# Kernel optimization log

Hardware: AMD Instinct MI355X
Metric: run time of the kernel (lower is better)

Reference implementation:

```python
import jax, jax.numpy as jnp
import numpy as np

NHEADS = 16
SCALE_BASE = 512
GN_EPS = 1e-5


def rotate_every_two(x):
    x1 = x[..., ::2]
    x2 = x[..., 1::2]
    return jnp.stack((-x2, x1), axis=-1).reshape(x.shape)


def xpos_apply(x, downscale, offset=0):
    # x: [B, T, C]; XPOS over the FULL embedding dim (applied before head split)
    B, T, C = x.shape
    half = C // 2
    scale_vec = (jnp.arange(0, C, 2, dtype=jnp.float32) + 0.4 * C) / (1.4 * C)  # [half]
    min_pos = -(T + offset) // 2
    max_pos = T + offset + min_pos
    power = jnp.arange(min_pos, max_pos, dtype=jnp.float32) / SCALE_BASE  # [L]
    scale = scale_vec[None, :] ** power[:, None]  # [L, half]
    L = scale.shape[0]
    inv_freq = 1.0 / (10000.0 ** (jnp.arange(half, dtype=jnp.float32) / half))
    sinusoid = jnp.arange(L, dtype=jnp.float32)[:, None] * inv_freq[None, :]  # [L, half]
    sin, cos = jnp.sin(sinusoid), jnp.cos(sinusoid)
    if L > T:
        scale, sin, cos = scale[-T:], sin[-T:], cos[-T:]
    if downscale:
        scale = 1.0 / scale
    sin = jnp.repeat(sin * scale, 2, axis=-1)  # [T, C] (duplicate_interleave)
    cos = jnp.repeat(cos * scale, 2, axis=-1)
    return x * cos + rotate_every_two(x) * sin


def decay_mask(nheads, T):
    gamma = 1.0 - 2.0 ** (-5.0 - jnp.arange(nheads, dtype=jnp.float32))  # [H]
    idx = jnp.arange(T)
    diff = idx[:, None] - idx[None, :]  # [T, T]
    keep = diff >= 0
    m = gamma[:, None, None] ** jnp.where(keep, diff, 0).astype(jnp.float32)
    return jnp.where(keep[None, :, :], m, 0.0)  # [H, T, T]


def setup_inputs() -> dict:
    key = jax.random.key(0)
    ks = jax.random.split(key, 6)
    B, T, C = 2, 2048, 1024
    w_std = 0.02
    return {
        "x": jax.random.normal(ks[0], (B, T, C), jnp.float32),
        "w_qkvff": jax.random.normal(ks[1], (5 * C, C), jnp.float32) * w_std,
        "w_gated": jax.random.normal(ks[2], (C, C), jnp.float32) * w_std,
        "b_gated": jnp.zeros((C,), jnp.float32),
        "w_proj": jax.random.normal(ks[3], (C, C), jnp.float32) * w_std,
        "b_proj": jnp.zeros((C,), jnp.float32),
        "gn_w": jnp.ones((C,), jnp.float32),
        "gn_b": jnp.zeros((C,), jnp.float32),
        "w_ff": jax.random.normal(ks[4], (C, 2 * C), jnp.float32) * w_std,
        "rms_w": jnp.ones((C,), jnp.float32),
    }


def reference(x, w_qkvff, w_gated, b_gated, w_proj, b_proj, gn_w, gn_b, w_ff, rms_w):
    B, T, C = x.shape
    H = NHEADS
    hd = C // H
    # RMSNorm: x / clamp(||x|| * C^-0.5, 1e-8) * w
    nrm = jnp.sqrt(jnp.sum(x * x, axis=-1, keepdims=True)) * (C ** -0.5)
    x_ = x / jnp.maximum(nrm, 1e-8) * rms_w
    # fused qkvff projection (Linear, no bias): [B,T,5C]
    qkvff = jnp.einsum('btc,oc->bto', x_, w_qkvff)
    q, k, v, ff = jnp.split(qkvff, [C, 2 * C, 3 * C], axis=-1)
    q = xpos_apply(q, downscale=False)
    k = xpos_apply(k, downscale=True)
    # split heads -> [B,H,T,hd]
    q = q.reshape(B, T, H, hd).transpose(0, 2, 1, 3)
    k = k.reshape(B, T, H, hd).transpose(0, 2, 1, 3)
    v = v.reshape(B, T, H, hd).transpose(0, 2, 1, 3)
    # parallel retention: decay-masked QK^T @ V
    scores = jnp.einsum('bhtd,bhsd->bhts', q, k) * (hd ** -0.5)
    scores = scores * decay_mask(H, T)[None]
    y = jnp.einsum('bhts,bhsd->bhtd', scores, v)  # [B,H,T,hd]
    # GroupNorm(H groups) applied over flattened (B*T, C)
    yg = y.transpose(0, 2, 1, 3).reshape(B * T, H, hd)
    mu = jnp.mean(yg, axis=-1, keepdims=True)
    var = jnp.mean((yg - mu) ** 2, axis=-1, keepdims=True)
    yg = (yg - mu) / jnp.sqrt(var + GN_EPS)
    y = yg.reshape(B * T, C) * gn_w + gn_b
    y = y.reshape(B, T, C)
    # gated SiLU on raw x (pre-norm), then output proj
    y = jax.nn.silu(jnp.einsum('btc,oc->bto', x, w_gated) + b_gated) * y
    y = jnp.einsum('btc,oc->bto', y, w_proj) + b_proj
    # gated FFN branch: exact (erf) GELU then Linear(2C->C, no bias)
    ff_out = jnp.einsum('bte,ce->btc', jax.nn.gelu(ff, approximate=False), w_ff)
    return x + ff_out + y
```

## Files before the change

kernel.cpp:

```cpp
#include <hip/hip_runtime.h>
#include <math.h>

#define B_  2
#define T_  2048
#define C_  1024
#define H_  16
#define FC_ 5120

typedef __attribute__((ext_vector_type(8))) short  s16x8;
typedef __attribute__((ext_vector_type(4))) float  f32x4;
typedef __attribute__((ext_vector_type(2))) unsigned short u16x2;
typedef __attribute__((ext_vector_type(4))) unsigned short u16x4;
typedef __attribute__((ext_vector_type(8))) unsigned short u16x8;

#define AS1 __attribute__((address_space(1)))
#define AS3 __attribute__((address_space(3)))

__device__ __forceinline__ ushort f2bf(float f) {
    union { float f; unsigned u; } v; v.f = f;
    unsigned r = v.u + 0x7FFFu + ((v.u >> 16) & 1u);
    return (ushort)(r >> 16);
}
__device__ __forceinline__ float bf2f(ushort u) {
    union { unsigned u; float f; } v; v.u = (unsigned)u << 16; return v.f;
}
__device__ __forceinline__ void gload16(const void* g, void* l) {
    __builtin_amdgcn_global_load_lds((const AS1 unsigned int*)g,
                                     (AS3 unsigned int*)l, 16, 0, 0);
}

__global__ __launch_bounds__(256) void cvt_all_kernel(
        const float* __restrict__ wq, const float* __restrict__ wg,
        const float* __restrict__ wp, const float* __restrict__ wf,
        const float* __restrict__ rms_w,
        ushort* __restrict__ wqb, ushort* __restrict__ wgb,
        ushort* __restrict__ wpb, ushort* __restrict__ wfb) {
    int i = blockIdx.x * 256 + threadIdx.x;
    const float* src; ushort* dst; int off; bool fold = false;
    if (i < 655360)       { src = wq; dst = wqb; off = i; fold = true; }
    else if (i < 786432)  { src = wg; dst = wgb; off = i - 655360; }
    else if (i < 917504)  { src = wp; dst = wpb; off = i - 786432; }
    else                  { src = wf; dst = wfb; off = i - 917504; }
    float4 a = ((const float4*)src)[2*off];
    float4 b = ((const float4*)src)[2*off + 1];
    if (fold) {
        int c = (off * 8) & 1023;
        float4 r0 = *(const float4*)(rms_w + c);
        float4 r1 = *(const float4*)(rms_w + c + 4);
        a.x *= r0.x; a.y *= r0.y; a.z *= r0.z; a.w *= r0.w;
        b.x *= r1.x; b.y *= r1.y; b.z *= r1.z; b.w *= r1.w;
    }
    u16x8 o;
    o[0] = f2bf(a.x); o[1] = f2bf(a.y); o[2] = f2bf(a.z); o[3] = f2bf(a.w);
    o[4] = f2bf(b.x); o[5] = f2bf(b.y); o[6] = f2bf(b.z); o[7] = f2bf(b.w);
    *(u16x8*)(dst + 8*off) = o;
}

__global__ __launch_bounds__(256) void rmsx_kernel(const float* __restrict__ x,
                                                   ushort* __restrict__ xb,
                                                   float* __restrict__ inv_out) {
    int row = blockIdx.x;
    int tid = threadIdx.x;
    float4 v = ((const float4*)(x + (size_t)row * C_))[tid];
    u16x4 o;
    o[0] = f2bf(v.x); o[1] = f2bf(v.y); o[2] = f2bf(v.z); o[3] = f2bf(v.w);
    *(u16x4*)(xb + (size_t)row * C_ + 4*tid) = o;
    float ss = v.x*v.x + v.y*v.y + v.z*v.z + v.w*v.w;
    #pragma unroll
    for (int m = 32; m >= 1; m >>= 1) ss += __shfl_xor(ss, m);
    __shared__ float wsum[4];
    if ((tid & 63) == 0) wsum[tid >> 6] = ss;
    __syncthreads();
    if (tid == 0) {
        float tot = wsum[0] + wsum[1] + wsum[2] + wsum[3];
        inv_out[row] = 1.0f / fmaxf(sqrtf(tot) * 0.03125f, 1e-8f);
    }
}

__global__ __launch_bounds__(256) void xpos_bf16_kernel(const ushort* __restrict__ qktmp,
                                                        ushort* __restrict__ qkv) {
    int bt = blockIdx.x;
    int t = bt & (T_ - 1);
    float tf = (float)t;
    const ushort* row = qktmp + (size_t)bt * 2048;
    ushort* orow = qkv + (size_t)bt * 3072;
    float power = (tf - 1024.0f) * (1.0f / 512.0f);
    for (int i = threadIdx.x; i < 512; i += 256) {
        float sv    = (2.0f * (float)i + 409.6f) * (1.0f / 1433.6f);
        float scale = exp2f(power * log2f(sv));
        float invf  = exp2f((float)i * (-13.287712379549449f / 512.0f));
        float ang   = tf * invf;
        float sn, cs;
        sincosf(ang, &sn, &cs);
        float rs = 1.0f / scale;
        int hh = i >> 5;
        float lg2g = log2f(1.0f - exp2f(-5.0f - (float)hh));
        float gq = exp2f(lg2g * tf) * 0.125f;
        float gk = exp2f(-lg2g * tf);
        u16x2 qi = *(const u16x2*)(row + 2*i);
        u16x2 ki = *(const u16x2*)(row + 1024 + 2*i);
        float qx = bf2f(qi[0]), qy = bf2f(qi[1]);
        float kx = bf2f(ki[0]), ky = bf2f(ki[1]);
        float qox = (qx*(cs*scale) - qy*(sn*scale)) * gq;
        float qoy = (qy*(cs*scale) + qx*(sn*scale)) * gq;
        float kox = (kx*(cs*rs) - ky*(sn*rs)) * gk;
        float koy = (ky*(cs*rs) + kx*(sn*rs)) * gk;
        u16x2 qo; qo[0] = f2bf(qox); qo[1] = f2bf(qoy);
        u16x2 ko; ko[0] = f2bf(kox); ko[1] = f2bf(koy);
        *(u16x2*)(orow + 2*i) = qo;
        *(u16x2*)(orow + 1024 + 2*i) = ko;
    }
}

template<int EPI, int BN>
__global__ __launch_bounds__(256) void gemm_bf16_kernel(
        const ushort* __restrict__ A, int lda,
        const ushort* __restrict__ W, int ldw,
        float* __restrict__ Cmat, int ldc, int K,
        const float* __restrict__ bias,
        const float* __restrict__ add1,
        const float* __restrict__ add2,
        const float* __restrict__ inv,
        ushort* __restrict__ oqk,
        ushort* __restrict__ ov,
        ushort* __restrict__ offb,
        ushort* __restrict__ ogate) {
    constexpr int NG = BN / 32;
    __shared__ __align__(16) ushort As[2][128*64];
    __shared__ __align__(16) ushort Bs[2][BN*64];
    int tid = threadIdx.x;
    int m0 = blockIdx.y * 128, n0 = blockIdx.x * BN;
    int wave = tid >> 6, lane = tid & 63;
    int lo = lane & 15, hi = lane >> 4;
    int wm = (wave >> 1) * 64, wn = (wave & 1) * (BN/2);
    int lrow  = lane >> 3;
    int gcol  = ((lane & 7) ^ lrow) * 8;
    f32x4 acc[4][NG] = {};

    auto stage = [&](int k0, int buf) {
        #pragma unroll
        for (int i = 0; i < 4; ++i) {
            int c = wave*4 + i;
            gload16(A + (size_t)(m0 + c*8 + lrow) * lda + k0 + gcol,
                    (ushort*)As[buf] + c*512);
        }
        if constexpr (BN == 128) {
            #pragma unroll
            for (int i = 0; i < 4; ++i) {
                int c = wave*4 + i;
                gload16(W + (size_t)(n0 + c*8 + lrow) * ldw + k0 + gcol,
                        (ushort*)Bs[buf] + c*512);
            }
        } else {
            #pragma unroll
            for (int i = 0; i < 2; ++i) {
                int c = wave*2 + i;
                gload16(W + (size_t)(n0 + c*8 + lrow) * ldw + k0 + gcol,
                        (ushort*)Bs[buf] + c*512);
            }
        }
    };

    int cur = 0;
    stage(0, 0);
    __syncthreads();
    for (int k0 = 0;;) {
        int nxt = k0 + 64;
        if (nxt < K) stage(nxt, cur ^ 1);
        #pragma unroll
        for (int kc = 0; kc < 2; ++kc) {
            s16x8 af[4], bf[NG];
            #pragma unroll
            for (int g = 0; g < 4; ++g) {
                int arow = wm + g*16 + lo;
                af[g] = *(const s16x8*)((const char*)As[cur] +
                         arow*128 + ((kc*64 + hi*16) ^ ((arow & 7) << 4)));
            }
            #pragma unroll
            for (int g = 0; g < NG; ++g) {
                int brow = wn + g*16 + lo;
                bf[g] = *(const s16x8*)((const char*)Bs[cur] +
                         brow*128 + ((kc*64 + hi*16) ^ ((brow & 7) << 4)));
            }
            #pragma unroll
            for (int mg = 0; mg < 4; ++mg)
                #pragma unroll
                for (int ng = 0; ng < NG; ++ng)
                    acc[mg][ng] = __builtin_amdgcn_mfma_f32_16x16x32_bf16(
                        af[mg], bf[ng], acc[mg][ng], 0, 0, 0);
        }
        if (nxt >= K) break;
        __syncthreads();
        cur ^= 1; k0 = nxt;
    }
    #pragma unroll
    for (int mg = 0; mg < 4; ++mg) {
        #pragma unroll
        for (int r = 0; r < 4; ++r) {
            size_t m = (size_t)(m0 + wm + mg*16 + hi*4 + r);
            float iv = 1.0f;
            if constexpr (EPI == 4) iv = inv[m];
            #pragma unroll
            for (int ng = 0; ng < NG; ++ng) {
                int n = n0 + wn + ng*16 + lo;
                float v = acc[mg][ng][r];
                if constexpr (EPI == 4) {
                    if (n0 < 2048)      oqk[m*2048 + n] = f2bf(v * iv);
                    else if (n0 < 3072) ov[m*3072 + n] = f2bf(v * iv);
                    else if (n0 < 5120) {
                        float g = v * iv;
                        offb[m*2048 + (n - 3072)] =
                            f2bf(0.5f * g * (1.0f + erff(g * 0.70710678118f)));
                    } else {
                        float s = v + bias[n - 5120];
                        ogate[m*1024 + (n - 5120)] = f2bf(s / (1.0f + expf(-s)));
                    }
                } else {
                    if (EPI == 2)
                        v += bias[n] + add1[m*ldc + n] + add2[m*ldc + n];
                    Cmat[m*ldc + n] = v;
                }
            }
        }
    }
}

__global__ __launch_bounds__(256) void attn_mfma2_kernel(const ushort* __restrict__ qkv,
                                                         float* __restrict__ y) {
    __shared__ ushort Ks[2][64*64];
    __shared__ ushort Vt[2][64*64];
    __shared__ ushort Ss[4][16*64];
    int F = blockIdx.x;
    int o = (F & 7) * 64 + (F >> 3);
    int tta = o & 15;
    int h   = (o >> 4) & 15;
    int b   = o >> 8;
    int ttb = 31 - tta;
    int t0a = tta * 64, t0b = ttb * 64;
    int tid = threadIdx.x;
    int wave = tid >> 6, lane = tid & 63;
    int lo = lane & 15, hi = lane >> 4;
    const size_t bT = (size_t)b * T_;

    const ushort* qra = qkv + (bT + t0a + wave*16 + lo) * 3072 + h*64;
    const ushort* qrb = qkv + (bT + t0b + wave*16 + lo) * 3072 + h*64;
    s16x8 qa0 = *(const s16x8*)(qra + hi*8);
    s16x8 qa1 = *(const s16x8*)(qra + 32 + hi*8);
    s16x8 qb0 = *(const s16x8*)(qrb + hi*8);
    s16x8 qb1 = *(const s16x8*)(qrb + 32 + hi*8);
    f32x4 acca[4] = {}, accb[4] = {};

    int kr = tid >> 2, kc = tid & 3;
    int vd0 = (tid & 15) * 4, vs0 = (tid >> 4) * 4;
    u16x8 rka, rkb;
    u16x4 rv0, rv1, rv2, rv3;
    auto loadt = [&](int s0) {
        const ushort* src = qkv + (bT + s0 + kr) * 3072 + 1024 + h*64;
        rka = *(const u16x8*)(src + kc*8);
        rkb = *(const u16x8*)(src + (kc+4)*8);
        const ushort* vsrc = qkv + (bT + s0 + vs0) * 3072 + 2048 + h*64 + vd0;
        rv0 = *(const u16x4*)(vsrc);
        rv1 = *(const u16x4*)(vsrc + 3072);
        rv2 = *(const u16x4*)(vsrc + 2*3072);
        rv3 = *(const u16x4*)(vsrc + 3*3072);
    };
    int cur = 0;
    loadt(0);
    for (int st = 0; st <= ttb; ++st) {
        {
            int base = kr * 128, sw = (kr & 7) << 4;
            *(u16x8*)((char*)Ks[cur] + ((base + kc*16) ^ sw))     = rka;
            *(u16x8*)((char*)Ks[cur] + ((base + (kc+4)*16) ^ sw)) = rkb;
            #pragma unroll
            for (int i = 0; i < 4; ++i) {
                u16x4 o4; o4[0] = rv0[i]; o4[1] = rv1[i]; o4[2] = rv2[i]; o4[3] = rv3[i];
                int d = vd0 + i;
                *(u16x4*)((char*)Vt[cur] + ((d*128 + vs0*2) ^ ((d & 7) << 4))) = o4;
            }
        }
        __syncthreads();
        if (st < ttb) loadt((st + 1) * 64);

        auto compute = [&](s16x8 q0, s16x8 q1, f32x4* accy, bool diag) {
            f32x4 sacc[4] = {};
            #pragma unroll
            for (int sn = 0; sn < 4; ++sn) {
                int srow = sn*16 + lo;
                int rb2 = srow * 128, sw = (srow & 7) << 4;
                s16x8 kf0 = *(const s16x8*)((const char*)Ks[cur] + ((rb2 + hi*16) ^ sw));
                s16x8 kf1 = *(const s16x8*)((const char*)Ks[cur] + ((rb2 + 64 + hi*16) ^ sw));
                sacc[sn] = __builtin_amdgcn_mfma_f32_16x16x32_bf16(q0, kf0, sacc[sn], 0, 0, 0);
                sacc[sn] = __builtin_amdgcn_mfma_f32_16x16x32_bf16(q1, kf1, sacc[sn], 0, 0, 0);
            }
            #pragma unroll
            for (int sn = 0; sn < 4; ++sn) {
                int sl = sn*16 + lo;
                #pragma unroll
                for (int r = 0; r < 4; ++r) {
                    float v = sacc[sn][r];
                    if (diag && sl > wave*16 + hi*4 + r) v = 0.0f;
                    int tq = hi*4 + r;
                    *(ushort*)((char*)Ss[wave] + ((tq*128 + sl*2) ^ ((tq & 7) << 4))) = f2bf(v);
                }
            }
            s16x8 sa0 = *(const s16x8*)((const char*)Ss[wave] + ((lo*128 + hi*16) ^ ((lo & 7) << 4)));
            s16x8 sa1 = *(const s16x8*)((const char*)Ss[wave] + ((lo*128 + 64 + hi*16) ^ ((lo & 7) << 4)));
            #pragma unroll
            for (int dn = 0; dn < 4; ++dn) {
                int d = dn*16 + lo;
                int rb2 = d * 128, sw = (d & 7) << 4;
                s16x8 vf0 = *(const s16x8*)((const char*)Vt[cur] + ((rb2 + hi*16) ^ sw));
                s16x8 vf1 = *(const s16x8*)((const char*)Vt[cur] + ((rb2 + 64 + hi*16) ^ sw));
                accy[dn] = __builtin_amdgcn_mfma_f32_16x16x32_bf16(sa0, vf0, accy[dn], 0, 0, 0);
                accy[dn] = __builtin_amdgcn_mfma_f32_16x16x32_bf16(sa1, vf1, accy[dn], 0, 0, 0);
            }
        };
        compute(qb0, qb1, accb, st == ttb);
        if (st <= tta) compute(qa0, qa1, acca, st == tta);
        cur ^= 1;
    }
    #pragma unroll
    for (int dn = 0; dn < 4; ++dn) {
        #pragma unroll
        for (int r = 0; r < 4; ++r) {
            int ta = t0a + wave*16 + hi*4 + r;
            int tb = t0b + wave*16 + hi*4 + r;
            y[(bT + ta) * C_ + h*64 + dn*16 + lo] = acca[dn][r];
            y[(bT + tb) * C_ + h*64 + dn*16 + lo] = accb[dn][r];
        }
    }
}

__global__ __launch_bounds__(256) void gn_gate_kernel(const float* __restrict__ y,
                                                      const ushort* __restrict__ gateb,
                                                      const float* __restrict__ gn_w,
                                                      const float* __restrict__ gn_b,
                                                      ushort* __restrict__ ygb) {
    int bt = blockIdx.x;
    int tid = threadIdx.x;
    float4 v = ((const float4*)(y + (size_t)bt * C_))[tid];
    float s1 = v.x + v.y + v.z + v.w;
    float s2 = v.x*v.x + v.y*v.y + v.z*v.z + v.w*v.w;
    #pragma unroll
    for (int m = 1; m < 16; m <<= 1) { s1 += __shfl_xor(s1, m); s2 += __shfl_xor(s2, m); }
    float mu   = s1 * (1.0f/64.0f);
    float var  = s2 * (1.0f/64.0f) - mu*mu;
    float rstd = rsqrtf(var + 1e-5f);
    float4 w  = ((const float4*)gn_w)[tid];
    float4 bb = ((const float4*)gn_b)[tid];
    u16x4 g4 = *(const u16x4*)(gateb + (size_t)bt * C_ + 4*tid);
    u16x4 o;
    o[0] = f2bf(((v.x - mu)*rstd*w.x + bb.x) * bf2f(g4[0]));
    o[1] = f2bf(((v.y - mu)*rstd*w.y + bb.y) * bf2f(g4[1]));
    o[2] = f2bf(((v.z - mu)*rstd*w.z + bb.z) * bf2f(g4[2]));
    o[3] = f2bf(((v.w - mu)*rstd*w.w + bb.w) * bf2f(g4[3]));
    *(u16x4*)(ygb + (size_t)bt * C_ + 4*tid) = o;
}

extern "C" void kernel_launch(void* const* d_in, const int* in_sizes, int n_in,
                              void* d_out, int out_size, void* d_ws, size_t ws_size,
                              hipStream_t stream) {
    (void)in_sizes; (void)n_in; (void)out_size; (void)ws_size;
    const float* x       = (const float*)d_in[0];
    const float* w_qkvff = (const float*)d_in[1];
    const float* w_gated = (const float*)d_in[2];
    const float* b_gated = (const float*)d_in[3];
    const float* w_proj  = (const float*)d_in[4];
    const float* b_proj  = (const float*)d_in[5];
    const float* gn_w    = (const float*)d_in[6];
    const float* gn_b    = (const float*)d_in[7];
    const float* w_ff    = (const float*)d_in[8];
    const float* rms_w   = (const float*)d_in[9];
    float* out = (float*)d_out;

    const size_t NTOK = (size_t)B_ * T_;
    float* buf0   = (float*)d_ws;
    float* buf1   = buf0 + NTOK * C_;
    ushort* qkvb  = (ushort*)(buf1 + NTOK * C_);
    ushort* qktmp = qkvb + NTOK * 3072;
    ushort* xb    = qktmp + NTOK * 2048;
    ushort* ffb   = xb + NTOK * C_;
    ushort* ygb   = ffb + NTOK * 2048;
    ushort* gateb = ygb + NTOK * C_;
    ushort* wqb   = gateb + NTOK * C_;
    ushort* wgb   = wqb + (size_t)FC_ * C_;
    ushort* wpb   = wgb + (size_t)C_ * C_;
    ushort* wfb   = wpb + (size_t)C_ * C_;
    float* inv    = (float*)(wfb + (size_t)C_ * 2*C_);

    cvt_all_kernel<<<4608, 256, 0, stream>>>(w_qkvff, w_gated, w_proj, w_ff, rms_w,
                                             wqb, wgb, wpb, wfb);
    rmsx_kernel<<<4096, 256, 0, stream>>>(x, xb, inv);
    gemm_bf16_kernel<4,128><<<dim3(48, 32), 256, 0, stream>>>(
        xb, C_, wqb, C_, nullptr, 0, C_, b_gated, nullptr, nullptr, inv,
        qktmp, qkvb, ffb, gateb);
    xpos_bf16_kernel<<<4096, 256, 0, stream>>>(qktmp, qkvb);
    attn_mfma2_kernel<<<512, 256, 0, stream>>>(qkvb, buf1);
    gn_gate_kernel<<<4096, 256, 0, stream>>>(buf1, gateb, gn_w, gn_b, ygb);
    gemm_bf16_kernel<0,64><<<dim3(16, 32), 256, 0, stream>>>(
        ffb, 2*C_, wfb, 2*C_, buf0, C_, 2*C_, nullptr, nullptr, nullptr, nullptr,
        nullptr, nullptr, nullptr, nullptr);
    gemm_bf16_kernel<2,64><<<dim3(16, 32), 256, 0, stream>>>(
        ygb, C_, wpb, C_, out, C_, C_, b_proj, x, buf0, nullptr,
        nullptr, nullptr, nullptr, nullptr);
}
```

Measured before the change: 350.2 us.

## Fuse XPOS rotation into QKV GEMM epilogue and drop LDS double buffering

Removes the separate xpos kernel and applies the rotary/XPOS scaling and decay factors inside the first GEMM's epilogue, using a lane shuffle to fetch the pair partner. This eliminates the intermediate qktmp buffer write/read and one kernel launch. It also changes all GEMMs from double-buffered LDS staging to single-buffered with two barriers per k-step, which reduces LDS use but serialises loads with MFMA work. The epilogue now computes transcendentals per element, which adds ALU work to the GEMM.

```diff
diff --git a/kernel.cpp b/kernel.cpp
--- a/kernel.cpp
+++ b/kernel.cpp
@@ -77,41 +77,6 @@
     }
 }
 
-__global__ __launch_bounds__(256) void xpos_bf16_kernel(const ushort* __restrict__ qktmp,
-                                                        ushort* __restrict__ qkv) {
-    int bt = blockIdx.x;
-    int t = bt & (T_ - 1);
-    float tf = (float)t;
-    const ushort* row = qktmp + (size_t)bt * 2048;
-    ushort* orow = qkv + (size_t)bt * 3072;
-    float power = (tf - 1024.0f) * (1.0f / 512.0f);
-    for (int i = threadIdx.x; i < 512; i += 256) {
-        float sv    = (2.0f * (float)i + 409.6f) * (1.0f / 1433.6f);
-        float scale = exp2f(power * log2f(sv));
-        float invf  = exp2f((float)i * (-13.287712379549449f / 512.0f));
-        float ang   = tf * invf;
-        float sn, cs;
-        sincosf(ang, &sn, &cs);
-        float rs = 1.0f / scale;
-        int hh = i >> 5;
-        float lg2g = log2f(1.0f - exp2f(-5.0f - (float)hh));
-        float gq = exp2f(lg2g * tf) * 0.125f;
-        float gk = exp2f(-lg2g * tf);
-        u16x2 qi = *(const u16x2*)(row + 2*i);
-        u16x2 ki = *(const u16x2*)(row + 1024 + 2*i);
-        float qx = bf2f(qi[0]), qy = bf2f(qi[1]);
-        float kx = bf2f(ki[0]), ky = bf2f(ki[1]);
-        float qox = (qx*(cs*scale) - qy*(sn*scale)) * gq;
-        float qoy = (qy*(cs*scale) + qx*(sn*scale)) * gq;
-        float kox = (kx*(cs*rs) - ky*(sn*rs)) * gk;
-        float koy = (ky*(cs*rs) + kx*(sn*rs)) * gk;
-        u16x2 qo; qo[0] = f2bf(qox); qo[1] = f2bf(qoy);
-        u16x2 ko; ko[0] = f2bf(kox); ko[1] = f2bf(koy);
-        *(u16x2*)(orow + 2*i) = qo;
-        *(u16x2*)(orow + 1024 + 2*i) = ko;
-    }
-}
-
 template<int EPI, int BN>
 __global__ __launch_bounds__(256) void gemm_bf16_kernel(
         const ushort* __restrict__ A, int lda,
@@ -121,13 +86,12 @@
         const float* __restrict__ add1,
         const float* __restrict__ add2,
         const float* __restrict__ inv,
-        ushort* __restrict__ oqk,
         ushort* __restrict__ ov,
         ushort* __restrict__ offb,
         ushort* __restrict__ ogate) {
     constexpr int NG = BN / 32;
-    __shared__ __align__(16) ushort As[2][128*64];
-    __shared__ __align__(16) ushort Bs[2][BN*64];
+    __shared__ __align__(16) ushort As[128*64];
+    __shared__ __align__(16) ushort Bs[BN*64];
     int tid = threadIdx.x;
     int m0 = blockIdx.y * 128, n0 = blockIdx.x * BN;
     int wave = tid >> 6, lane = tid & 63;
@@ -137,49 +101,43 @@
     int gcol  = ((lane & 7) ^ lrow) * 8;
     f32x4 acc[4][NG] = {};
 
-    auto stage = [&](int k0, int buf) {
+    for (int k0 = 0; k0 < K; k0 += 64) {
+        __syncthreads();
         #pragma unroll
         for (int i = 0; i < 4; ++i) {
             int c = wave*4 + i;
             gload16(A + (size_t)(m0 + c*8 + lrow) * lda + k0 + gcol,
-                    (ushort*)As[buf] + c*512);
+                    (ushort*)As + c*512);
         }
         if constexpr (BN == 128) {
             #pragma unroll
             for (int i = 0; i < 4; ++i) {
                 int c = wave*4 + i;
                 gload16(W + (size_t)(n0 + c*8 + lrow) * ldw + k0 + gcol,
-                        (ushort*)Bs[buf] + c*512);
+                        (ushort*)Bs + c*512);
             }
         } else {
             #pragma unroll
             for (int i = 0; i < 2; ++i) {
                 int c = wave*2 + i;
                 gload16(W + (size_t)(n0 + c*8 + lrow) * ldw + k0 + gcol,
-                        (ushort*)Bs[buf] + c*512);
-            }
-        }
-    };
-
-    int cur = 0;
-    stage(0, 0);
-    __syncthreads();
-    for (int k0 = 0;;) {
-        int nxt = k0 + 64;
-        if (nxt < K) stage(nxt, cur ^ 1);
+                        (ushort*)Bs + c*512);
+            }
+        }
+        __syncthreads();
         #pragma unroll
         for (int kc = 0; kc < 2; ++kc) {
             s16x8 af[4], bf[NG];
             #pragma unroll
             for (int g = 0; g < 4; ++g) {
                 int arow = wm + g*16 + lo;
-                af[g] = *(const s16x8*)((const char*)As[cur] +
+                af[g] = *(const s16x8*)((const char*)As +
                          arow*128 + ((kc*64 + hi*16) ^ ((arow & 7) << 4)));
             }
             #pragma unroll
             for (int g = 0; g < NG; ++g) {
                 int brow = wn + g*16 + lo;
-                bf[g] = *(const s16x8*)((const char*)Bs[cur] +
+                bf[g] = *(const s16x8*)((const char*)Bs +
                          brow*128 + ((kc*64 + hi*16) ^ ((brow & 7) << 4)));
             }
             #pragma unroll
@@ -189,25 +147,42 @@
                     acc[mg][ng] = __builtin_amdgcn_mfma_f32_16x16x32_bf16(
                         af[mg], bf[ng], acc[mg][ng], 0, 0, 0);
         }
-        if (nxt >= K) break;
-        __syncthreads();
-        cur ^= 1; k0 = nxt;
     }
     #pragma unroll
     for (int mg = 0; mg < 4; ++mg) {
         #pragma unroll
         for (int r = 0; r < 4; ++r) {
             size_t m = (size_t)(m0 + wm + mg*16 + hi*4 + r);
-            float iv = 1.0f;
-            if constexpr (EPI == 4) iv = inv[m];
+            float iv = 1.0f, tf = 0.0f, power = 0.0f;
+            if constexpr (EPI == 4) {
+                iv = inv[m];
+                tf = (float)(int)(m & (T_ - 1));
+                power = (tf - 1024.0f) * (1.0f / 512.0f);
+            }
             #pragma unroll
             for (int ng = 0; ng < NG; ++ng) {
                 int n = n0 + wn + ng*16 + lo;
                 float v = acc[mg][ng][r];
                 if constexpr (EPI == 4) {
-                    if (n0 < 2048)      oqk[m*2048 + n] = f2bf(v * iv);
-                    else if (n0 < 3072) ov[m*3072 + n] = f2bf(v * iv);
-                    else if (n0 < 5120) {
+                    if (n0 < 2048) {
+                        float q = v * iv;
+                        float p = __shfl_xor(q, 1);
+                        int c = n & 1023;
+                        int ip = c >> 1;
+                        float sv    = (2.0f*(float)ip + 409.6f) * (1.0f/1433.6f);
+                        float scale = exp2f(power * log2f(sv));
+                        float invf  = exp2f((float)ip * (-13.287712379549449f/512.0f));
+                        float sn, cs;
+                        sincosf(tf * invf, &sn, &cs);
+                        float rot = (n & 1) ? (q*cs + p*sn) : (q*cs - p*sn);
+                        float lg2g = log2f(1.0f - exp2f(-5.0f - (float)(c >> 6)));
+                        float gsc, ssc;
+                        if (n0 < 1024) { gsc = exp2f(lg2g*tf) * 0.125f; ssc = scale; }
+                        else           { gsc = exp2f(-lg2g*tf); ssc = 1.0f/scale; }
+                        ov[m*3072 + n] = f2bf(rot * ssc * gsc);
+                    } else if (n0 < 3072) {
+                        ov[m*3072 + n] = f2bf(v * iv);
+                    } else if (n0 < 5120) {
                         float g = v * iv;
                         offb[m*2048 + (n - 3072)] =
                             f2bf(0.5f * g * (1.0f + erff(g * 0.70710678118f)));
@@ -377,8 +352,7 @@
     float* buf0   = (float*)d_ws;
     float* buf1   = buf0 + NTOK * C_;
     ushort* qkvb  = (ushort*)(buf1 + NTOK * C_);
-    ushort* qktmp = qkvb + NTOK * 3072;
-    ushort* xb    = qktmp + NTOK * 2048;
+    ushort* xb    = qkvb + NTOK * 3072;
     ushort* ffb   = xb + NTOK * C_;
     ushort* ygb   = ffb + NTOK * 2048;
     ushort* gateb = ygb + NTOK * C_;
@@ -393,14 +367,13 @@
     rmsx_kernel<<<4096, 256, 0, stream>>>(x, xb, inv);
     gemm_bf16_kernel<4,128><<<dim3(48, 32), 256, 0, stream>>>(
         xb, C_, wqb, C_, nullptr, 0, C_, b_gated, nullptr, nullptr, inv,
-        qktmp, qkvb, ffb, gateb);
-    xpos_bf16_kernel<<<4096, 256, 0, stream>>>(qktmp, qkvb);
+        qkvb, ffb, gateb);
     attn_mfma2_kernel<<<512, 256, 0, stream>>>(qkvb, buf1);
     gn_gate_kernel<<<4096, 256, 0, stream>>>(buf1, gateb, gn_w, gn_b, ygb);
     gemm_bf16_kernel<0,64><<<dim3(16, 32), 256, 0, stream>>>(
         ffb, 2*C_, wfb, 2*C_, buf0, C_, 2*C_, nullptr, nullptr, nullptr, nullptr,
-        nullptr, nullptr, nullptr, nullptr);
+        nullptr, nullptr, nullptr);
     gemm_bf16_kernel<2,64><<<dim3(16, 32), 256, 0, stream>>>(
         ygb, C_, wpb, C_, out, C_, C_, b_proj, x, buf0, nullptr,
-        nullptr, nullptr, nullptr, nullptr);
-}
+        nullptr, nullptr, nullptr);
+}
```

Measured after the change: 805.8 us. 130% more time.
